# Performance work log

Hardware: AMD Instinct MI355X
Metric: run time of the kernel (lower is better)

## Reference

```python
import jax, jax.numpy as jnp
import numpy as np

IN_DIM, HIDDEN_DIM, OUT_DIM = 128, 256, 128
N_NODES, N_EDGES = 100000, 1000000


def setup_inputs() -> dict:
    key = jax.random.key(0)
    ks = jax.random.split(key, 8)
    s = lambda d: 1.0 / np.sqrt(d)
    x = jax.random.normal(ks[0], (N_NODES, IN_DIM), dtype=jnp.float32)
    edge_index = jax.random.randint(ks[1], (2, N_EDGES), 0, N_NODES, dtype=jnp.int64)
    # encoder: Linear(in,hid) -> ReLU -> Linear(hid,out)
    W1 = jax.random.uniform(ks[2], (IN_DIM, HIDDEN_DIM), jnp.float32, -s(IN_DIM), s(IN_DIM))
    b1 = jnp.zeros((HIDDEN_DIM,), jnp.float32)
    W2 = jax.random.uniform(ks[3], (HIDDEN_DIM, OUT_DIM), jnp.float32, -s(HIDDEN_DIM), s(HIDDEN_DIM))
    b2 = jnp.zeros((OUT_DIM,), jnp.float32)
    # pred: Linear(2*out,hid) -> ReLU -> Linear(hid,1)
    W3 = jax.random.uniform(ks[4], (2 * OUT_DIM, HIDDEN_DIM), jnp.float32, -s(2 * OUT_DIM), s(2 * OUT_DIM))
    b3 = jnp.zeros((HIDDEN_DIM,), jnp.float32)
    W4 = jax.random.uniform(ks[5], (HIDDEN_DIM, 1), jnp.float32, -s(HIDDEN_DIM), s(HIDDEN_DIM))
    b4 = jnp.zeros((1,), jnp.float32)
    return {"x": x, "edge_index": edge_index, "W1": W1, "b1": b1, "W2": W2,
            "b2": b2, "W3": W3, "b3": b3, "W4": W4, "b4": b4}


def reference(x, edge_index, W1, b1, W2, b2, W3, b3, W4, b4):
    # node encoder
    h = jax.nn.relu(x @ W1 + b1) @ W2 + b2            # [N, out_dim]
    # edge gather + concat
    h_src = h[edge_index[0]]                          # [E, out_dim]
    h_dst = h[edge_index[1]]                          # [E, out_dim]
    e = jnp.concatenate([h_src, h_dst], axis=-1)      # [E, 2*out_dim]
    # edge predictor
    logits = jax.nn.relu(e @ W3 + b3) @ W4 + b4       # [E, 1]
    return jax.nn.sigmoid(logits)
```

## Files before the change

### kernel.cpp

```cpp
#include <hip/hip_runtime.h>


#define NN 100000
#define NE 1000000
#define NTN 1563
#define GRID_EP 2048

typedef __attribute__((ext_vector_type(8))) __bf16 bf16x8;
typedef __attribute__((ext_vector_type(4))) float f32x4;
typedef __attribute__((ext_vector_type(4))) unsigned short us4;

__device__ __forceinline__ unsigned short f2bf(float f) {
    unsigned u = __float_as_uint(f);
    return (unsigned short)((u + 0x7FFFu + ((u >> 16) & 1u)) >> 16);
}
__device__ __forceinline__ float bflo(unsigned w) {
    return __uint_as_float(w << 16);
}
__device__ __forceinline__ float bfhi(unsigned w) {
    return __uint_as_float(w & 0xffff0000u);
}

template <int CTRL>
__device__ __forceinline__ float dpp_add(float v) {
    return v + __int_as_float(__builtin_amdgcn_update_dpp(
                   0, __float_as_int(v), CTRL, 0xF, 0xF, true));
}
__device__ __forceinline__ float row_reduce16(float v) {
    v = dpp_add<0x118>(v);
    v = dpp_add<0x114>(v);
    v = dpp_add<0x112>(v);
    v = dpp_add<0x111>(v);
    return v;
}

__global__ void prep1(const float* __restrict__ W1, const float* __restrict__ W2,
                      const float* __restrict__ W3, const float* __restrict__ b2,
                      const float* __restrict__ b3, const float* __restrict__ W4,
                      const void* __restrict__ eidx,
                      unsigned short* __restrict__ w1s,
                      unsigned short* __restrict__ wuts,
                      unsigned short* __restrict__ wvts, float* __restrict__ bu,
                      float* __restrict__ bv, float* __restrict__ w4p,
                      int* __restrict__ flag) {
    int t = blockIdx.x * blockDim.x + threadIdx.x;
    if (t < 32768) {
        int k = t >> 8, n = t & 255;
        w1s[(k >> 3) * 2048 + n * 8 + (k & 7)] = f2bf(W1[t]);
    }
    if (t < 65536) {
        int k = t >> 8, n = t & 255;
        float s = 0.0f;
        for (int j = 0; j < 128; ++j) s += W2[k * 128 + j] * W3[j * 256 + n];
        wuts[(k >> 3) * 2048 + n * 8 + (k & 7)] = f2bf(s);
    } else {
        int i = t - 65536;
        int k = i >> 8, n = i & 255;
        float s = 0.0f;
        for (int j = 0; j < 128; ++j) s += W2[k * 128 + j] * W3[(128 + j) * 256 + n];
        wvts[(k >> 3) * 2048 + n * 8 + (k & 7)] = f2bf(s);
    }
    if (t < 256) {
        float s = b3[t];
        for (int j = 0; j < 128; ++j) s += b2[j] * W3[j * 256 + t];
        bu[t] = s;
    } else if (t < 512) {
        int n = t - 256;
        float s = 0.0f;
        for (int j = 0; j < 128; ++j) s += b2[j] * W3[(128 + j) * 256 + n];
        bv[n] = s;
    } else if (t < 768) {
        int p = t - 512;
        int wq = p >> 6, local = p & 63;
        w4p[p] = W4[wq * 64 + (local & 3) * 16 + ((local >> 2) & 15)];
    }
    if (t == 0) {
        const unsigned* u = (const unsigned*)eidx;
        int all0 = 1;
        for (int i = 0; i < 32; ++i) all0 &= (u[2 * i + 1] == 0u);
        *flag = all0;
    }
}

__global__ __launch_bounds__(256, 3) void node_uv(
    const float* __restrict__ x, const float* __restrict__ b1,
    const unsigned short* __restrict__ w1s, const unsigned short* __restrict__ wuts,
    const unsigned short* __restrict__ wvts, const float* __restrict__ bu,
    const float* __restrict__ bv, unsigned short* __restrict__ Ug,
    unsigned short* __restrict__ Vg) {
    __shared__ __align__(16) unsigned short A1[64 * 136];
    __shared__ __align__(16) unsigned short A2[64 * 264];

    const int t = threadIdx.x, lane = t & 63, w = t >> 6;
    const int cl = lane & 15, q = lane >> 4;
    const int nb = w * 64;
    const int m0 = blockIdx.x * 64;

    {
        const float4* x4 = (const float4*)x;
#pragma unroll
        for (int i = 0; i < 8; ++i) {
            int lin = i * 256 + t;
            int m = lin >> 5, c = lin & 31;
            int node = m0 + m;
            if (node > NN - 1) node = NN - 1;
            float4 v = x4[node * 32 + c];
            us4 b;
            b.x = f2bf(v.x); b.y = f2bf(v.y); b.z = f2bf(v.z); b.w = f2bf(v.w);
            *(us4*)(A1 + m * 136 + c * 4) = b;
        }
    }
    float b1v[4], buv[4], bvv[4];
#pragma unroll
    for (int nt = 0; nt < 4; ++nt) {
        int n = nb + nt * 16 + cl;
        b1v[nt] = b1[n];
        buv[nt] = bu[n];
        bvv[nt] = bv[n];
    }
    __syncthreads();

    {
        f32x4 acc[4][4];
#pragma unroll
        for (int mt = 0; mt < 4; ++mt)
#pragma unroll
            for (int nt = 0; nt < 4; ++nt)
                acc[mt][nt] = (f32x4){b1v[nt], b1v[nt], b1v[nt], b1v[nt]};
#pragma unroll
        for (int s = 0; s < 4; ++s) {
            bf16x8 a[4], bw[4];
#pragma unroll
            for (int mt = 0; mt < 4; ++mt)
                a[mt] = *(const bf16x8*)(A1 + (mt * 16 + cl) * 136 + s * 32 + q * 8);
#pragma unroll
            for (int nt = 0; nt < 4; ++nt)
                bw[nt] = *(const bf16x8*)(w1s + (s * 4 + q) * 2048 +
                                          (nb + nt * 16 + cl) * 8);
#pragma unroll
            for (int mt = 0; mt < 4; ++mt)
#pragma unroll
                for (int nt = 0; nt < 4; ++nt)
                    acc[mt][nt] = __builtin_amdgcn_mfma_f32_16x16x32_bf16(
                        a[mt], bw[nt], acc[mt][nt], 0, 0, 0);
        }
#pragma unroll
        for (int mt = 0; mt < 4; ++mt)
#pragma unroll
            for (int nt = 0; nt < 4; ++nt)
#pragma unroll
                for (int r = 0; r < 4; ++r) {
                    float v = fmaxf(acc[mt][nt][r], 0.0f);
                    A2[(mt * 16 + q * 4 + r) * 264 + nb + nt * 16 + cl] = f2bf(v);
                }
    }
    __syncthreads();

#pragma unroll
    for (int pass = 0; pass < 2; ++pass) {
        const unsigned short* wt = pass ? wvts : wuts;
        unsigned short* outg = pass ? Vg : Ug;
        f32x4 acc[4][4];
#pragma unroll
        for (int mt = 0; mt < 4; ++mt)
#pragma unroll
            for (int nt = 0; nt < 4; ++nt) {
                float bb = pass ? bvv[nt] : buv[nt];
                acc[mt][nt] = (f32x4){bb, bb, bb, bb};
            }
#pragma unroll
        for (int s = 0; s < 8; ++s) {
            bf16x8 a[4], bw[4];
#pragma unroll
            for (int mt = 0; mt < 4; ++mt)
                a[mt] = *(const bf16x8*)(A2 + (mt * 16 + cl) * 264 + s * 32 + q * 8);
#pragma unroll
            for (int nt = 0; nt < 4; ++nt)
                bw[nt] = *(const bf16x8*)(wt + (s * 4 + q) * 2048 +
                                          (nb + nt * 16 + cl) * 8);
#pragma unroll
            for (int mt = 0; mt < 4; ++mt)
#pragma unroll
                for (int nt = 0; nt < 4; ++nt)
                    acc[mt][nt] = __builtin_amdgcn_mfma_f32_16x16x32_bf16(
                        a[mt], bw[nt], acc[mt][nt], 0, 0, 0);
        }
#pragma unroll
        for (int mt = 0; mt < 4; ++mt)
#pragma unroll
            for (int r = 0; r < 4; ++r) {
                int node = m0 + mt * 16 + q * 4 + r;
                if (node < NN) {
                    us4 v = {f2bf(acc[mt][0][r]), f2bf(acc[mt][1][r]),
                             f2bf(acc[mt][2][r]), f2bf(acc[mt][3][r])};
                    *(us4*)(outg + node * 256 + nb + cl * 4) = v;
                }
            }
    }
}

#define TERM(uw, vw, wa, wb)                                     \
    (fmaxf(bflo(uw) + bflo(vw), 0.0f) * (wa) +                   \
     fmaxf(bfhi(uw) + bfhi(vw), 0.0f) * (wb))

__global__ __launch_bounds__(256, 8) void edge_pred(
    const void* __restrict__ eidx, const unsigned short* __restrict__ Ut,
    const unsigned short* __restrict__ Vt, const float* __restrict__ w4p,
    const float* __restrict__ b4, const int* __restrict__ flag,
    float* __restrict__ out) {
    const int t = threadIdx.x, lane = t & 63;
    const int cl = lane & 15, g = lane >> 4;
    const int gwid = (blockIdx.x * 256 + t) >> 6;
    const int nw = (GRID_EP * 256) >> 6;
    const bool i64f = (*flag != 0);
    const int* ei32 = (const int*)eidx;
    const long long* ei64 = (const long long*)eidx;

    float w4a[8], w4b[8];
#pragma unroll
    for (int j = 0; j < 8; ++j) {
        w4a[j] = w4p[cl * 8 + j];
        w4b[j] = w4p[128 + cl * 8 + j];
    }
    const float b4v = b4[0];

    for (int base = gwid * 8; base < NE; base += nw * 8) {
        const int eA = base + g, eB = base + 4 + g;
        int sA = i64f ? (int)ei64[eA] : ei32[eA];
        int dA = i64f ? (int)ei64[NE + eA] : ei32[NE + eA];
        int sB = i64f ? (int)ei64[eB] : ei32[eB];
        int dB = i64f ? (int)ei64[NE + eB] : ei32[NE + eB];
        sA = sA < 0 ? 0 : (sA > NN - 1 ? NN - 1 : sA);
        dA = dA < 0 ? 0 : (dA > NN - 1 ? NN - 1 : dA);
        sB = sB < 0 ? 0 : (sB > NN - 1 ? NN - 1 : sB);
        dB = dB < 0 ? 0 : (dB > NN - 1 ? NN - 1 : dB);

        const uint4* ua = (const uint4*)(Ut + (long)sA * 256) + cl;
        const uint4* va = (const uint4*)(Vt + (long)dA * 256) + cl;
        const uint4* ub = (const uint4*)(Ut + (long)sB * 256) + cl;
        const uint4* vb = (const uint4*)(Vt + (long)dB * 256) + cl;
        uint4 ua0 = ua[0], ua1 = ua[16];
        uint4 va0 = va[0], va1 = va[16];
        uint4 ub0 = ub[0], ub1 = ub[16];
        uint4 vb0 = vb[0], vb1 = vb[16];

        float accA =
            TERM(ua0.x, va0.x, w4a[0], w4a[1]) + TERM(ua0.y, va0.y, w4a[2], w4a[3]) +
            TERM(ua0.z, va0.z, w4a[4], w4a[5]) + TERM(ua0.w, va0.w, w4a[6], w4a[7]) +
            TERM(ua1.x, va1.x, w4b[0], w4b[1]) + TERM(ua1.y, va1.y, w4b[2], w4b[3]) +
            TERM(ua1.z, va1.z, w4b[4], w4b[5]) + TERM(ua1.w, va1.w, w4b[6], w4b[7]);
        float accB =
            TERM(ub0.x, vb0.x, w4a[0], w4a[1]) + TERM(ub0.y, vb0.y, w4a[2], w4a[3]) +
            TERM(ub0.z, vb0.z, w4a[4], w4a[5]) + TERM(ub0.w, vb0.w, w4a[6], w4a[7]) +
            TERM(ub1.x, vb1.x, w4b[0], w4b[1]) + TERM(ub1.y, vb1.y, w4b[2], w4b[3]) +
            TERM(ub1.z, vb1.z, w4b[4], w4b[5]) + TERM(ub1.w, vb1.w, w4b[6], w4b[7]);

        accA = row_reduce16(accA);
        accB = row_reduce16(accB);
        if (cl == 15) {
            out[eA] = 1.0f / (1.0f + __expf(-(accA + b4v)));
            out[eB] = 1.0f / (1.0f + __expf(-(accB + b4v)));
        }
    }
}

extern "C" void kernel_launch(void* const* d_in, const int* in_sizes, int n_in,
                              void* d_out, int out_size, void* d_ws, size_t ws_size,
                              hipStream_t stream) {
    const float* x  = (const float*)d_in[0];
    const void*  ei = d_in[1];
    const float* W1 = (const float*)d_in[2];
    const float* b1 = (const float*)d_in[3];
    const float* W2 = (const float*)d_in[4];
    const float* b2 = (const float*)d_in[5];
    const float* W3 = (const float*)d_in[6];
    const float* b3 = (const float*)d_in[7];
    const float* W4 = (const float*)d_in[8];
    const float* b4 = (const float*)d_in[9];

    char* ws = (char*)d_ws;
    int* flag            = (int*)ws;
    unsigned short* w1s  = (unsigned short*)(ws + 256);
    unsigned short* wuts = (unsigned short*)(ws + 65792);
    unsigned short* wvts = (unsigned short*)(ws + 196864);
    float* bu            = (float*)(ws + 327936);
    float* bv            = (float*)(ws + 328960);
    float* w4p           = (float*)(ws + 329984);
    unsigned short* Ug   = (unsigned short*)(ws + 1048576);
    unsigned short* Vg   = (unsigned short*)(ws + 52248576);

    prep1<<<512, 256, 0, stream>>>(W1, W2, W3, b2, b3, W4, ei, w1s, wuts, wvts,
                                   bu, bv, w4p, flag);
    node_uv<<<NTN, 256, 0, stream>>>(x, b1, w1s, wuts, wvts, bu, bv, Ug, Vg);
    edge_pred<<<GRID_EP, 256, 0, stream>>>(ei, Ug, Vg, w4p, b4, flag, (float*)d_out);
}
```

Baseline: 296.8 us.

## Stage second-layer weights in LDS and alias A1 onto A2 in node_uv

The node_uv kernel now cooperatively copies each 16K-element quarter of the Wu/Wv weight matrices into a shared LDS buffer before the MFMA loop. All waves then read B fragments from LDS instead of each wave loading them directly from global memory. A1 is aliased onto A2 to free LDS for the new buffer, and the first-layer results are written to A2 only after a barrier. Launch bounds drop from 3 to 2 blocks per SM, and the extra barriers per quarter may limit overlap.

Result: slower. 305.9 us (+3.1%).

```diff
diff --git a/kernel.cpp b/kernel.cpp
--- a/kernel.cpp
+++ b/kernel.cpp
@@ -82,14 +82,15 @@
     }
 }
 
-__global__ __launch_bounds__(256, 3) void node_uv(
+__global__ __launch_bounds__(256, 2) void node_uv(
     const float* __restrict__ x, const float* __restrict__ b1,
     const unsigned short* __restrict__ w1s, const unsigned short* __restrict__ wuts,
     const unsigned short* __restrict__ wvts, const float* __restrict__ bu,
     const float* __restrict__ bv, unsigned short* __restrict__ Ug,
     unsigned short* __restrict__ Vg) {
-    __shared__ __align__(16) unsigned short A1[64 * 136];
     __shared__ __align__(16) unsigned short A2[64 * 264];
+    __shared__ __align__(16) unsigned short Bbuf[16384];
+    unsigned short* A1 = A2;
 
     const int t = threadIdx.x, lane = t & 63, w = t >> 6;
     const int cl = lane & 15, q = lane >> 4;
@@ -120,41 +121,40 @@
     }
     __syncthreads();
 
-    {
-        f32x4 acc[4][4];
+    f32x4 accg[4][4];
+#pragma unroll
+    for (int mt = 0; mt < 4; ++mt)
+#pragma unroll
+        for (int nt = 0; nt < 4; ++nt)
+            accg[mt][nt] = (f32x4){b1v[nt], b1v[nt], b1v[nt], b1v[nt]};
+#pragma unroll
+    for (int s = 0; s < 4; ++s) {
+        bf16x8 a[4], bw[4];
 #pragma unroll
         for (int mt = 0; mt < 4; ++mt)
+            a[mt] = *(const bf16x8*)(A1 + (mt * 16 + cl) * 136 + s * 32 + q * 8);
+#pragma unroll
+        for (int nt = 0; nt < 4; ++nt)
+            bw[nt] = *(const bf16x8*)(w1s + (s * 4 + q) * 2048 +
+                                      (nb + nt * 16 + cl) * 8);
+#pragma unroll
+        for (int mt = 0; mt < 4; ++mt)
 #pragma unroll
             for (int nt = 0; nt < 4; ++nt)
-                acc[mt][nt] = (f32x4){b1v[nt], b1v[nt], b1v[nt], b1v[nt]};
-#pragma unroll
-        for (int s = 0; s < 4; ++s) {
-            bf16x8 a[4], bw[4];
-#pragma unroll
-            for (int mt = 0; mt < 4; ++mt)
-                a[mt] = *(const bf16x8*)(A1 + (mt * 16 + cl) * 136 + s * 32 + q * 8);
-#pragma unroll
-            for (int nt = 0; nt < 4; ++nt)
-                bw[nt] = *(const bf16x8*)(w1s + (s * 4 + q) * 2048 +
-                                          (nb + nt * 16 + cl) * 8);
-#pragma unroll
-            for (int mt = 0; mt < 4; ++mt)
-#pragma unroll
-                for (int nt = 0; nt < 4; ++nt)
-                    acc[mt][nt] = __builtin_amdgcn_mfma_f32_16x16x32_bf16(
-                        a[mt], bw[nt], acc[mt][nt], 0, 0, 0);
-        }
-#pragma unroll
-        for (int mt = 0; mt < 4; ++mt)
-#pragma unroll
-            for (int nt = 0; nt < 4; ++nt)
-#pragma unroll
-                for (int r = 0; r < 4; ++r) {
-                    float v = fmaxf(acc[mt][nt][r], 0.0f);
-                    A2[(mt * 16 + q * 4 + r) * 264 + nb + nt * 16 + cl] = f2bf(v);
-                }
+                accg[mt][nt] = __builtin_amdgcn_mfma_f32_16x16x32_bf16(
+                    a[mt], bw[nt], accg[mt][nt], 0, 0, 0);
     }
     __syncthreads();
+
+#pragma unroll
+    for (int mt = 0; mt < 4; ++mt)
+#pragma unroll
+        for (int nt = 0; nt < 4; ++nt)
+#pragma unroll
+            for (int r = 0; r < 4; ++r) {
+                float v = fmaxf(accg[mt][nt][r], 0.0f);
+                A2[(mt * 16 + q * 4 + r) * 264 + nb + nt * 16 + cl] = f2bf(v);
+            }
 
 #pragma unroll
     for (int pass = 0; pass < 2; ++pass) {
@@ -169,21 +169,37 @@
                 acc[mt][nt] = (f32x4){bb, bb, bb, bb};
             }
 #pragma unroll
-        for (int s = 0; s < 8; ++s) {
-            bf16x8 a[4], bw[4];
-#pragma unroll
-            for (int mt = 0; mt < 4; ++mt)
-                a[mt] = *(const bf16x8*)(A2 + (mt * 16 + cl) * 264 + s * 32 + q * 8);
-#pragma unroll
-            for (int nt = 0; nt < 4; ++nt)
-                bw[nt] = *(const bf16x8*)(wt + (s * 4 + q) * 2048 +
-                                          (nb + nt * 16 + cl) * 8);
-#pragma unroll
-            for (int mt = 0; mt < 4; ++mt)
+        for (int qtr = 0; qtr < 4; ++qtr) {
+            {
+                const uint4* src = (const uint4*)(wt + qtr * 16384);
+                uint4* dst = (uint4*)Bbuf;
+#pragma unroll
+                for (int it = 0; it < 8; ++it) {
+                    int idx = it * 256 + t;
+                    dst[idx] = src[idx];
+                }
+            }
+            __syncthreads();
+#pragma unroll
+            for (int sh = 0; sh < 2; ++sh) {
+                const int s = qtr * 2 + sh;
+                bf16x8 a[4], bw[4];
+#pragma unroll
+                for (int mt = 0; mt < 4; ++mt)
+                    a[mt] = *(const bf16x8*)(A2 + (mt * 16 + cl) * 264 +
+                                             s * 32 + q * 8);
 #pragma unroll
                 for (int nt = 0; nt < 4; ++nt)
-                    acc[mt][nt] = __builtin_amdgcn_mfma_f32_16x16x32_bf16(
-                        a[mt], bw[nt], acc[mt][nt], 0, 0, 0);
+                    bw[nt] = *(const bf16x8*)(Bbuf + (sh * 4 + q) * 2048 +
+                                              (nb + nt * 16 + cl) * 8);
+#pragma unroll
+                for (int mt = 0; mt < 4; ++mt)
+#pragma unroll
+                    for (int nt = 0; nt < 4; ++nt)
+                        acc[mt][nt] = __builtin_amdgcn_mfma_f32_16x16x32_bf16(
+                            a[mt], bw[nt], acc[mt][nt], 0, 0, 0);
+            }
+            __syncthreads();
         }
 #pragma unroll
         for (int mt = 0; mt < 4; ++mt)
```
